# Performance work log

Measured on AMD Instinct MI355X. Metric: run time of the kernel, lower is better.

The kernel has to match this reference:

```python
import jax, jax.numpy as jnp
import numpy as np
from jax import lax

B, N, M = 4, 16384, 512
RADIUS2 = 4.0        # radius=2 (hard-coded in forward), compare squared distances
BALL_K = 64          # k=64 hard-coded in forward
KNN_K = 9            # opt.node_knn_k_1
SIGMA_LB = 0.001     # opt.loss_sigma_lower_bound

_DIMS = [("conv1", 6, 64), ("conv2", 64, 64), ("conv3", 64, 64),
         ("conv4", 128, 128), ("conv5", 128, 128),
         ("knnb1", 131, 256), ("knnb2", 256, 256), ("knnb3", 256, 256),
         ("knna1", 512, 512), ("knna2", 512, 512),
         ("mlp1", 640, 512), ("mlp2", 512, 256)]


def setup_inputs() -> dict:
    key = jax.random.key(0)
    ks = jax.random.split(key, 6)
    inp = {
        "x": jax.random.normal(ks[0], (B, 3, N), jnp.float32),
        "sn": jax.random.normal(ks[1], (B, 3, N), jnp.float32),
        "node": jax.random.normal(ks[2], (B, 3, M), jnp.float32),
    }
    for i, (name, cin, cout) in enumerate(_DIMS):
        k = jax.random.fold_in(ks[3], i)
        inp[name + "_w"] = jax.random.normal(k, (cout, cin), jnp.float32) * np.float32(1.0 / np.sqrt(cin))
        inp[name + "_b"] = jnp.zeros((cout,), jnp.float32)
    inp["mlp3_w"] = jax.random.normal(ks[4], (4, 256), jnp.float32) * np.float32(1e-4)  # .normal_(0, 0.0001)
    inp["mlp3_b"] = jnp.zeros((4,), jnp.float32)
    return inp


def _conv(f, w, b, act=True):
    # 1x1 conv over (B,C,M) or (B,C,M,K): channel matmul + bias (+relu)
    y = jnp.einsum('oc,bc...->bo...', w, f) + b.reshape((1, -1) + (1,) * (f.ndim - 2))
    return jax.nn.relu(y) if act else y


def _sqdist(a, b):
    # a: (B,3,Ma), b: (B,3,Nb) -> (B,Ma,Nb) squared euclidean distances
    aa = jnp.sum(a * a, axis=1)
    bb = jnp.sum(b * b, axis=1)
    ab = jnp.einsum('bcm,bcn->bmn', a, b)
    return aa[:, :, None] + bb[:, None, :] - 2.0 * ab


def _gather(feat, idx):
    # feat: (B,C,Nb), idx: (B,Mq,K) -> (B,C,Mq,K)
    Bq, C, _ = feat.shape
    _, Mq, K = idx.shape
    flat = jnp.broadcast_to(idx.reshape(Bq, 1, Mq * K), (Bq, C, Mq * K))
    return jnp.take_along_axis(feat, flat, axis=2).reshape(Bq, C, Mq, K)


def _ball_query(sqd, radius2, k):
    # first k point indices (in original order) with dist<radius, padded by the first hit
    n = sqd.shape[2]
    mask = sqd < radius2
    keyi = jnp.where(mask, jnp.arange(n, dtype=jnp.int32)[None, None, :], jnp.int32(n))
    _, idx = lax.top_k(-keyi, k)  # k smallest keys == first k in-ball indices
    count = jnp.sum(mask, axis=2, keepdims=True)
    return jnp.where(jnp.arange(k)[None, None, :] < count, idx, idx[:, :, :1])


def reference(x, sn, node,
              conv1_w, conv1_b, conv2_w, conv2_b, conv3_w, conv3_b,
              conv4_w, conv4_b, conv5_w, conv5_b,
              knnb1_w, knnb1_b, knnb2_w, knnb2_b, knnb3_w, knnb3_b,
              knna1_w, knna1_b, knna2_w, knna2_b,
              mlp1_w, mlp1_b, mlp2_w, mlp2_b, mlp3_w, mlp3_b):
    x_aug = jnp.concatenate([x, sn], axis=1)                      # (B,6,N)
    idx = _ball_query(_sqdist(node, x), RADIUS2, BALL_K)          # (B,M,64)
    xb = _gather(x_aug, idx)                                      # (B,6,M,64)
    xb = jnp.concatenate([xb[:, :3] - node[:, :, :, None], xb[:, 3:]], axis=1)
    f = _conv(_conv(_conv(xb, conv1_w, conv1_b), conv2_w, conv2_b), conv3_w, conv3_b)
    fmax = jnp.max(f, axis=3, keepdims=True)
    f = jnp.concatenate([f, jnp.broadcast_to(fmax, f.shape)], axis=1)
    f = _conv(_conv(f, conv4_w, conv4_b), conv5_w, conv5_b)
    feat1 = jnp.max(f, axis=3)                                    # (B,128,M)

    # GeneralKNNFusionModule: query=node, database=node, x=feat1, K=KNN_K
    _, knn_idx = lax.top_k(-_sqdist(node, node), KNN_K)           # (B,M,K) nearest nodes
    coords = _gather(node, knn_idx) - node[:, :, :, None]         # (B,3,M,K)
    g = jnp.concatenate([coords, _gather(feat1, knn_idx)], axis=1)  # (B,131,M,K)
    g = _conv(_conv(_conv(g, knnb1_w, knnb1_b), knnb2_w, knnb2_b), knnb3_w, knnb3_b)
    gmax = jnp.max(g, axis=3, keepdims=True)
    g = jnp.concatenate([g, jnp.broadcast_to(gmax, g.shape)], axis=1)
    g = _conv(_conv(g, knna1_w, knna1_b), knna2_w, knna2_b)
    feat2 = jnp.max(g, axis=3)                                    # (B,512,M)

    h = jnp.concatenate([feat1, feat2], axis=1)                   # (B,640,M)
    h = _conv(_conv(h, mlp1_w, mlp1_b), mlp2_w, mlp2_b)
    ksig = _conv(h, mlp3_w, mlp3_b, act=False)                    # (B,4,M)
    keypoints = ksig[:, :3] + node
    sigmas = jax.nn.softplus(ksig[:, 3]) + SIGMA_LB
    return node, keypoints, sigmas
```

## Files before the change

### kernel.cpp

```cpp
#include <hip/hip_runtime.h>

typedef unsigned short u16;
typedef unsigned int u32;
typedef __bf16 bf16x8 __attribute__((ext_vector_type(8)));
typedef float floatx4 __attribute__((ext_vector_type(4)));
typedef unsigned short u16x8 __attribute__((ext_vector_type(8)));
typedef unsigned int u32x4 __attribute__((ext_vector_type(4)));

static constexpr int B_ = 4;
static constexpr int N_ = 16384;
static constexpr int M_ = 512;

__device__ __forceinline__ u16 f2bf(float f) {
    u32 u = __float_as_uint(f);
    u32 r = (u + 0x7fffu + ((u >> 16) & 1u)) >> 16;
    return (u16)r;
}
__device__ __forceinline__ float bf2f(u16 x) {
    return __uint_as_float(((u32)x) << 16);
}
__device__ __forceinline__ u32 pack2(float a, float b) {
    return (u32)f2bf(a) | ((u32)f2bf(b) << 16);
}

__global__ void pack_x_kernel(const float* __restrict__ x, float4* __restrict__ pk) {
    int t = blockIdx.x * 256 + threadIdx.x;
    int b = t >> 14, n = t & (N_ - 1);
    const float* xb = x + (size_t)b * 3 * N_;
    float px = xb[n], py = xb[N_ + n], pz = xb[2 * N_ + n];
    pk[t] = make_float4(px, py, pz, px * px + py * py + pz * pz);
}

__global__ __launch_bounds__(256) void ball_query_kernel(
    const float4* __restrict__ pk, const float* __restrict__ node, int* __restrict__ idx) {
    int bm = blockIdx.x;
    int b = bm >> 9, m = bm & 511;
    int tid = threadIdx.x, wave = tid >> 6, lane = tid & 63;
    __shared__ int sidx[4][64];
    __shared__ int scnt[4];

    const float4* pb = pk + ((size_t)b << 14);
    float nx = node[((size_t)b * 3 + 0) * M_ + m];
    float ny = node[((size_t)b * 3 + 1) * M_ + m];
    float nz = node[((size_t)b * 3 + 2) * M_ + m];
    float aa = nx * nx + ny * ny + nz * nz;

    int cnt = 0;
    int base = wave * 4096;
    for (int n0 = base; n0 < base + 4096; n0 += 64) {
        float4 p = pb[n0 + lane];
        float d = aa + p.w - 2.0f * (nx * p.x + ny * p.y + nz * p.z);
        bool inb = d < 4.0f;
        unsigned long long mask = __ballot(inb);
        if (inb && cnt < 64) {
            int pos = cnt + __popcll(mask & ((1ull << lane) - 1ull));
            if (pos < 64) sidx[wave][pos] = n0 + lane;
        }
        cnt += __popcll(mask);
        if (cnt >= 64) break;
    }
    if (lane == 0) scnt[wave] = cnt;
    __syncthreads();
    if (tid < 64) {
        int total = scnt[0] + scnt[1] + scnt[2] + scnt[3];
        int v = 0;
        if (total > 0) {
            int lim = total < 64 ? total : 64;
            int slot = tid < lim ? tid : 0;
            int w = 0, pre = 0;
            while (w < 3 && slot >= pre + scnt[w]) { pre += scnt[w]; ++w; }
            v = sidx[w][slot - pre];
        }
        idx[(size_t)bm * 64 + tid] = v;
    }
}

__global__ void knn_kernel(const float* __restrict__ node, int* __restrict__ knn) {
    int bm = blockIdx.x;
    int b = bm >> 9, m = bm & 511;
    int lane = threadIdx.x;
    const float* nb = node + (size_t)b * 3 * M_;
    float nx = nb[m], ny = nb[M_ + m], nz = nb[2 * M_ + m];
    float aa = nx * nx + ny * ny + nz * nz;

    float dist[8];
    int didx[8];
#pragma unroll
    for (int i = 0; i < 8; ++i) {
        int n = lane + i * 64;
        float px = nb[n], py = nb[M_ + n], pz = nb[2 * M_ + n];
        float bb = px * px + py * py + pz * pz;
        float ab = nx * px + ny * py + nz * pz;
        dist[i] = aa + bb - 2.0f * ab;
        didx[i] = n;
    }
    for (int r = 0; r < 9; ++r) {
        float bv = dist[0]; int bi = didx[0]; int bslot = 0;
#pragma unroll
        for (int i = 1; i < 8; ++i) {
            if (dist[i] < bv || (dist[i] == bv && didx[i] < bi)) {
                bv = dist[i]; bi = didx[i]; bslot = i;
            }
        }
        float rv = bv; int ri = bi;
        for (int off = 32; off > 0; off >>= 1) {
            float ov = __shfl_down(rv, off);
            int   oi = __shfl_down(ri, off);
            if (ov < rv || (ov == rv && oi < ri)) { rv = ov; ri = oi; }
        }
        ri = __shfl(ri, 0);
        if (lane == 0) knn[(size_t)bm * 9 + r] = ri;
        if (bi == ri) dist[bslot] = 3.0e38f;
    }
}

struct WConvArgs { const float* src[12]; };

__global__ void convert_weights_kernel(WConvArgs args, u16* __restrict__ dst) {
    const int CI[12] = {6, 64, 64, 128, 128, 131, 256, 256, 512, 512, 640, 512};
    const int KP[12] = {32, 64, 64, 128, 128, 160, 256, 256, 512, 512, 640, 512};
    const int OFF[13] = {0, 2048, 6144, 10240, 26624, 43008, 83968, 149504,
                         215040, 477184, 739328, 1067008, 1198080};
    int e = blockIdx.x * 256 + threadIdx.x;
    if (e >= 1198080) return;
    int w = 0;
    while (e >= OFF[w + 1]) ++w;
    int local = e - OFF[w];
    int kp = KP[w];
    int co = local / kp, k = local - co * kp;
    float v = 0.0f;
    if (w == 5) {
        if (k < 3) v = args.src[5][(size_t)co * 131 + k];
        else if (k >= 8 && k < 136) v = args.src[5][(size_t)co * 131 + (k - 5)];
    } else if (k < CI[w]) {
        v = args.src[w][(size_t)co * CI[w] + k];
    }
    dst[e] = f2bf(v);
}

static constexpr int RS = 136;

__device__ __forceinline__ bf16x8 ldsA(const u16* act, int rf, int l15, int quad, int ks) {
    return *(const bf16x8*)(act + (rf * 16 + l15) * RS + ks * 32 + quad * 8);
}
__device__ __forceinline__ bf16x8 ldW(const u16* W, int ks, int l15, int quad, int kstride) {
    return *(const bf16x8*)(W + (size_t)l15 * kstride + ks * 32 + quad * 8);
}

__global__ __launch_bounds__(256, 2) void fused_stage1_kernel(
    const float* __restrict__ x, const float* __restrict__ sn,
    const float* __restrict__ node, const int* __restrict__ idx,
    const u16* __restrict__ Wbf,
    const float* __restrict__ b1, const float* __restrict__ b2,
    const float* __restrict__ b3, const float* __restrict__ b4,
    const float* __restrict__ b5, u16* __restrict__ h) {
    __shared__ __align__(16) u16 act[128 * RS];
    __shared__ __align__(16) u16 mv[2][64];
    int blk = blockIdx.x;
    int bm0 = blk * 2;
    int tid = threadIdx.x, wave = tid >> 6, lane = tid & 63;
    int quad = lane >> 4, l15 = lane & 15;

    {
        int row = tid & 127, grp = tid >> 7;
        int bm = bm0 + (row >> 6);
        int b = bm >> 9, m = bm & 511;
        int j = idx[(size_t)bm * 64 + (row & 63)];
        const float* xb = x + (size_t)b * 3 * N_;
        const float* sb = sn + (size_t)b * 3 * N_;
        u16* r = act + row * RS;
        if (grp == 0) {
            float c0 = xb[j]          - node[((size_t)b * 3 + 0) * M_ + m];
            float c1 = xb[N_ + j]     - node[((size_t)b * 3 + 1) * M_ + m];
            float c2 = xb[2 * N_ + j] - node[((size_t)b * 3 + 2) * M_ + m];
            *(u32*)(r)     = pack2(c0, c1);
            *(u32*)(r + 2) = pack2(c2, sb[j]);
        } else {
            *(u32*)(r + 4) = pack2(sb[N_ + j], sb[2 * N_ + j]);
            *(u32*)(r + 6) = 0u;
            u32x4* z = (u32x4*)(r + 8);
            z[0] = (u32x4){0u, 0u, 0u, 0u};
            z[1] = (u32x4){0u, 0u, 0u, 0u};
            z[2] = (u32x4){0u, 0u, 0u, 0u};
        }
    }
    __syncthreads();

    {
        const u16* Wp = Wbf + (size_t)(wave * 16) * 32;
        bf16x8 bw = ldW(Wp, 0, l15, quad, 32);
        floatx4 c[8];
#pragma unroll
        for (int rf = 0; rf < 8; ++rf) {
            bf16x8 a = ldsA(act, rf, l15, quad, 0);
            c[rf] = __builtin_amdgcn_mfma_f32_16x16x32_bf16(a, bw, (floatx4){0.f,0.f,0.f,0.f}, 0, 0, 0);
        }
        float bias = b1[wave * 16 + l15];
        __syncthreads();
#pragma unroll
        for (int rf = 0; rf < 8; ++rf)
#pragma unroll
            for (int r = 0; r < 4; ++r)
                act[(rf * 16 + quad * 4 + r) * RS + wave * 16 + l15] = f2bf(fmaxf(c[rf][r] + bias, 0.0f));
        __syncthreads();
    }

    const int WOFF23[2] = {2048, 6144};
    const float* bp23[2] = {b2, b3};
#pragma unroll 1
    for (int cv = 0; cv < 2; ++cv) {
        const u16* Wp = Wbf + WOFF23[cv] + (size_t)(wave * 16) * 64;
        bf16x8 bw0 = ldW(Wp, 0, l15, quad, 64);
        bf16x8 bw1 = ldW(Wp, 1, l15, quad, 64);
        floatx4 c[8] = {};
#pragma unroll
        for (int ks = 0; ks < 2; ++ks)
#pragma unroll
            for (int rf = 0; rf < 8; ++rf) {
                bf16x8 a = ldsA(act, rf, l15, quad, ks);
                c[rf] = __builtin_amdgcn_mfma_f32_16x16x32_bf16(a, ks ? bw1 : bw0, c[rf], 0, 0, 0);
            }
        float bias = bp23[cv][wave * 16 + l15];
        float mxA = 0.0f, mxB = 0.0f;
#pragma unroll
        for (int rf = 0; rf < 8; ++rf)
#pragma unroll
            for (int r = 0; r < 4; ++r) {
                float v = fmaxf(c[rf][r] + bias, 0.0f);
                if (rf < 4) mxA = fmaxf(mxA, v); else mxB = fmaxf(mxB, v);
            }
        __syncthreads();
#pragma unroll
        for (int rf = 0; rf < 8; ++rf)
#pragma unroll
            for (int r = 0; r < 4; ++r)
                act[(rf * 16 + quad * 4 + r) * RS + wave * 16 + l15] = f2bf(fmaxf(c[rf][r] + bias, 0.0f));
        if (cv == 1) {
            mxA = fmaxf(mxA, __shfl_xor(mxA, 16));
            mxA = fmaxf(mxA, __shfl_xor(mxA, 32));
            mxB = fmaxf(mxB, __shfl_xor(mxB, 16));
            mxB = fmaxf(mxB, __shfl_xor(mxB, 32));
            if (quad == 0) {
                mv[0][wave * 16 + l15] = f2bf(mxA);
                mv[1][wave * 16 + l15] = f2bf(mxB);
            }
        }
        __syncthreads();
    }

    {
        const u16* Wp = Wbf + 10240 + (size_t)(wave * 32) * 128;
        bf16x8 bw[2][4];
#pragma unroll
        for (int cf = 0; cf < 2; ++cf)
#pragma unroll
            for (int ks = 0; ks < 4; ++ks)
                bw[cf][ks] = ldW(Wp + (size_t)cf * 16 * 128, ks, l15, quad, 128);
        floatx4 c[8][2] = {};
#pragma unroll
        for (int ks = 0; ks < 4; ++ks)
#pragma unroll
            for (int rf = 0; rf < 8; ++rf) {
                bf16x8 a = (ks < 2) ? ldsA(act, rf, l15, quad, ks)
                                    : *(const bf16x8*)(&mv[rf >> 2][(ks - 2) * 32 + quad * 8]);
#pragma unroll
                for (int cf = 0; cf < 2; ++cf)
                    c[rf][cf] = __builtin_amdgcn_mfma_f32_16x16x32_bf16(a, bw[cf][ks], c[rf][cf], 0, 0, 0);
            }
        float bias[2];
#pragma unroll
        for (int cf = 0; cf < 2; ++cf) bias[cf] = b4[wave * 32 + cf * 16 + l15];
        __syncthreads();
#pragma unroll
        for (int rf = 0; rf < 8; ++rf)
#pragma unroll
            for (int cf = 0; cf < 2; ++cf)
#pragma unroll
                for (int r = 0; r < 4; ++r)
                    act[(rf * 16 + quad * 4 + r) * RS + wave * 32 + cf * 16 + l15] =
                        f2bf(fmaxf(c[rf][cf][r] + bias[cf], 0.0f));
        __syncthreads();
    }

    {
        const u16* Wp = Wbf + 26624 + (size_t)(wave * 32) * 128;
        bf16x8 bw[2][4];
#pragma unroll
        for (int cf = 0; cf < 2; ++cf)
#pragma unroll
            for (int ks = 0; ks < 4; ++ks)
                bw[cf][ks] = ldW(Wp + (size_t)cf * 16 * 128, ks, l15, quad, 128);
        floatx4 c[8][2] = {};
#pragma unroll
        for (int ks = 0; ks < 4; ++ks)
#pragma unroll
            for (int rf = 0; rf < 8; ++rf) {
                bf16x8 a = ldsA(act, rf, l15, quad, ks);
#pragma unroll
                for (int cf = 0; cf < 2; ++cf)
                    c[rf][cf] = __builtin_amdgcn_mfma_f32_16x16x32_bf16(a, bw[cf][ks], c[rf][cf], 0, 0, 0);
            }
#pragma unroll
        for (int cf = 0; cf < 2; ++cf) {
            float bias = b5[wave * 32 + cf * 16 + l15];
            float mxA = 0.0f, mxB = 0.0f;
#pragma unroll
            for (int rf = 0; rf < 8; ++rf)
#pragma unroll
                for (int r = 0; r < 4; ++r) {
                    float v = fmaxf(c[rf][cf][r] + bias, 0.0f);
                    if (rf < 4) mxA = fmaxf(mxA, v); else mxB = fmaxf(mxB, v);
                }
            mxA = fmaxf(mxA, __shfl_xor(mxA, 16));
            mxA = fmaxf(mxA, __shfl_xor(mxA, 32));
            mxB = fmaxf(mxB, __shfl_xor(mxB, 16));
            mxB = fmaxf(mxB, __shfl_xor(mxB, 32));
            if (quad == 0) {
                h[(size_t)bm0 * 640 + wave * 32 + cf * 16 + l15] = f2bf(mxA);
                h[(size_t)(bm0 + 1) * 640 + wave * 32 + cf * 16 + l15] = f2bf(mxB);
            }
        }
    }
}

template <int KS, int CF, int RF, int RSx>
__device__ __forceinline__ void conv_inplace(u16* act, const u16* __restrict__ W0, int KP,
                                             const float* __restrict__ bias, int cb,
                                             int l15, int quad) {
    floatx4 acc[RF][CF];
#pragma unroll
    for (int rf = 0; rf < RF; ++rf)
#pragma unroll
        for (int cf = 0; cf < CF; ++cf) acc[rf][cf] = (floatx4){0.f, 0.f, 0.f, 0.f};

    bf16x8 bwA[CF], bwB[CF];
#pragma unroll
    for (int cf = 0; cf < CF; ++cf)
        bwA[cf] = *(const bf16x8*)(W0 + (size_t)(cb + cf * 16 + l15) * KP + quad * 8);

#pragma unroll
    for (int ks = 0; ks < KS; ++ks) {
        bf16x8* cur = (ks % 2 == 0) ? bwA : bwB;
        bf16x8* nxt = (ks % 2 == 0) ? bwB : bwA;
        if (ks + 1 < KS) {
#pragma unroll
            for (int cf = 0; cf < CF; ++cf)
                nxt[cf] = *(const bf16x8*)(W0 + (size_t)(cb + cf * 16 + l15) * KP +
                                           (ks + 1) * 32 + quad * 8);
        }
#pragma unroll
        for (int rf = 0; rf < RF; ++rf) {
            bf16x8 a = *(const bf16x8*)(act + (rf * 16 + l15) * RSx + ks * 32 + quad * 8);
#pragma unroll
            for (int cf = 0; cf < CF; ++cf)
                acc[rf][cf] = __builtin_amdgcn_mfma_f32_16x16x32_bf16(a, cur[cf], acc[rf][cf], 0, 0, 0);
        }
    }
    __syncthreads();
#pragma unroll
    for (int cf = 0; cf < CF; ++cf) {
        float bs = bias[cb + cf * 16 + l15];
#pragma unroll
        for (int rf = 0; rf < RF; ++rf)
#pragma unroll
            for (int r = 0; r < 4; ++r)
                act[(rf * 16 + quad * 4 + r) * RSx + cb + cf * 16 + l15] =
                    f2bf(fmaxf(acc[rf][cf][r] + bs, 0.0f));
    }
    __syncthreads();
}

static constexpr int RS2 = 520;

__global__ __launch_bounds__(1024, 4) void fused_stage2_kernel(
    const float* __restrict__ node, u16* __restrict__ h, const int* __restrict__ knn,
    const u16* __restrict__ Wbf,
    const float* __restrict__ bb1, const float* __restrict__ bb2,
    const float* __restrict__ bb3, const float* __restrict__ ba1,
    const float* __restrict__ ba2) {
    __shared__ __align__(16) u16 act[80 * RS2];
    int blk = blockIdx.x;
    int node0 = blk * 8;
    int b = node0 >> 9;
    int tid = threadIdx.x, wave = tid >> 6, lane = tid & 63;
    int quad = lane >> 4, l15 = lane & 15;
    (void)lane;

    for (int e = tid; e < 80 * 20; e += 1024)
        *(u16x8*)(act + (e / 20) * RS2 + (e % 20) * 8) = (u16x8){0,0,0,0,0,0,0,0};
    __syncthreads();
    for (int e = tid; e < 72 * 3; e += 1024) {
        int r = e / 3, c = e - r * 3;
        int nodei = node0 + r / 9;
        int j = knn[(size_t)nodei * 9 + (r % 9)];
        float v = node[((size_t)b * 3 + c) * M_ + j] - node[((size_t)b * 3 + c) * M_ + (nodei & 511)];
        act[r * RS2 + c] = f2bf(v);
    }
    for (int e = tid; e < 72 * 16; e += 1024) {
        int r = e >> 4, s = e & 15;
        int nodei = node0 + r / 9;
        int j = knn[(size_t)nodei * 9 + (r % 9)];
        *(u16x8*)(act + r * RS2 + 8 + s * 8) =
            *(const u16x8*)(h + (size_t)(b * 512 + j) * 640 + s * 8);
    }
    __syncthreads();

    conv_inplace<5, 1, 5, RS2>(act, Wbf + 43008, 160, bb1, wave * 16, l15, quad);
    conv_inplace<8, 1, 5, RS2>(act, Wbf + 83968, 256, bb2, wave * 16, l15, quad);
    conv_inplace<8, 1, 5, RS2>(act, Wbf + 149504, 256, bb3, wave * 16, l15, quad);

    for (int e = tid; e < 8 * 32; e += 1024) {
        int li = e >> 5, s = e & 31;
        int r0 = li * 9;
        float mx[8];
#pragma unroll
        for (int i = 0; i < 8; ++i) mx[i] = -3.0e38f;
#pragma unroll
        for (int kk = 0; kk < 9; ++kk) {
            u16x8 v = *(const u16x8*)(act + (r0 + kk) * RS2 + s * 8);
#pragma unroll
            for (int i = 0; i < 8; ++i) mx[i] = fmaxf(mx[i], bf2f(v[i]));
        }
        u16x8 o;
#pragma unroll
        for (int i = 0; i < 8; ++i) o[i] = f2bf(mx[i]);
#pragma unroll
        for (int kk = 0; kk < 9; ++kk)
            *(u16x8*)(act + (r0 + kk) * RS2 + 256 + s * 8) = o;
    }
    __syncthreads();

    conv_inplace<16, 2, 5, RS2>(act, Wbf + 215040, 512, ba1, wave * 32, l15, quad);
    conv_inplace<16, 2, 5, RS2>(act, Wbf + 477184, 512, ba2, wave * 32, l15, quad);

    for (int e = tid; e < 8 * 64; e += 1024) {
        int li = e >> 6, s = e & 63;
        int r0 = li * 9;
        float mx[8];
#pragma unroll
        for (int i = 0; i < 8; ++i) mx[i] = -3.0e38f;
#pragma unroll
        for (int kk = 0; kk < 9; ++kk) {
            u16x8 v = *(const u16x8*)(act + (r0 + kk) * RS2 + s * 8);
#pragma unroll
            for (int i = 0; i < 8; ++i) mx[i] = fmaxf(mx[i], bf2f(v[i]));
        }
        u16x8 o;
#pragma unroll
        for (int i = 0; i < 8; ++i) o[i] = f2bf(mx[i]);
        *(u16x8*)(h + (size_t)(node0 + li) * 640 + 128 + s * 8) = o;
    }
}

static constexpr int RS3 = 648;

__global__ __launch_bounds__(512, 2) void fused_stage3_kernel(
    const float* __restrict__ node, const u16* __restrict__ h,
    const u16* __restrict__ Wbf,
    const float* __restrict__ bm1, const float* __restrict__ bm2,
    const float* __restrict__ w3, const float* __restrict__ b3,
    float* __restrict__ out) {
    __shared__ __align__(16) u16 act[16 * RS3];
    int blk = blockIdx.x;
    int node0 = blk * 8;
    int tid = threadIdx.x, lane = tid & 63, wave = tid >> 6;
    int quad = lane >> 4, l15 = lane & 15;

    for (int e = tid; e < 16 * 80; e += 512) {
        int r = e / 80, seg = e - r * 80;
        u16x8 v = (r < 8) ? *(const u16x8*)(h + (size_t)(node0 + r) * 640 + seg * 8)
                          : (u16x8){0,0,0,0,0,0,0,0};
        *(u16x8*)(act + r * RS3 + seg * 8) = v;
    }
    __syncthreads();

    conv_inplace<20, 4, 1, RS3>(act, Wbf + 739328, 640, bm1, wave * 64, l15, quad);
    conv_inplace<16, 2, 1, RS3>(act, Wbf + 1067008, 512, bm2, wave * 32, l15, quad);

    if (tid < 32) {
        int li = tid >> 2, oc = tid & 3;
        const u16* row = act + li * RS3;
        const float* wrow = w3 + oc * 256;
        float a = 0.0f;
        for (int c = 0; c < 256; c += 4) {
            a += bf2f(row[c]) * wrow[c];
            a += bf2f(row[c + 1]) * wrow[c + 1];
            a += bf2f(row[c + 2]) * wrow[c + 2];
            a += bf2f(row[c + 3]) * wrow[c + 3];
        }
        a += b3[oc];
        int nodei = node0 + li;
        int b = nodei >> 9, m = nodei & 511;
        if (oc < 3) {
            float nv = node[((size_t)b * 3 + oc) * M_ + m];
            out[((size_t)b * 3 + oc) * M_ + m] = nv;
            out[6144 + ((size_t)b * 3 + oc) * M_ + m] = nv + a;
        } else {
            out[12288 + nodei] = fmaxf(a, 0.0f) + log1pf(expf(-fabsf(a))) + 0.001f;
        }
    }
}

extern "C" void kernel_launch(void* const* d_in, const int* in_sizes, int n_in,
                              void* d_out, int out_size, void* d_ws, size_t ws_size,
                              hipStream_t stream) {
    (void)in_sizes; (void)n_in; (void)out_size; (void)ws_size;
    const float* x = (const float*)d_in[0];
    const float* sn = (const float*)d_in[1];
    const float* node = (const float*)d_in[2];
    const float* W[13];
    const float* Bs[13];
    for (int i = 0; i < 13; ++i) {
        W[i] = (const float*)d_in[3 + 2 * i];
        Bs[i] = (const float*)d_in[4 + 2 * i];
    }
    float* out = (float*)d_out;

    char* ws = (char*)d_ws;
    int* idx = (int*)(ws + 0);
    int* knn = (int*)(ws + 524288);
    u16* Wbf = (u16*)(ws + 598016);
    u16* h   = (u16*)(ws + 2994176);
    float4* pk = (float4*)(ws + 5615616);

    WConvArgs wa;
    for (int w = 0; w < 12; ++w) wa.src[w] = W[w];
    convert_weights_kernel<<<(1198080 + 255) / 256, 256, 0, stream>>>(wa, Wbf);

    pack_x_kernel<<<256, 256, 0, stream>>>(x, pk);
    ball_query_kernel<<<2048, 256, 0, stream>>>(pk, node, idx);
    knn_kernel<<<2048, 64, 0, stream>>>(node, knn);

    fused_stage1_kernel<<<1024, 256, 0, stream>>>(x, sn, node, idx, Wbf,
                                                  Bs[0], Bs[1], Bs[2], Bs[3], Bs[4], h);
    fused_stage2_kernel<<<256, 1024, 0, stream>>>(node, h, knn, Wbf,
                                                  Bs[5], Bs[6], Bs[7], Bs[8], Bs[9]);
    fused_stage3_kernel<<<256, 512, 0, stream>>>(node, h, Wbf, Bs[10], Bs[11],
                                                 W[12], Bs[12], out);
}
```

Before: 257.6 us.

## Merge preprocessing kernels into one launch and deepen weight prefetch pipeline

```diff
diff --git a/kernel.cpp b/kernel.cpp
--- a/kernel.cpp
+++ b/kernel.cpp
@@ -23,119 +23,110 @@
     return (u32)f2bf(a) | ((u32)f2bf(b) << 16);
 }
 
-__global__ void pack_x_kernel(const float* __restrict__ x, float4* __restrict__ pk) {
-    int t = blockIdx.x * 256 + threadIdx.x;
-    int b = t >> 14, n = t & (N_ - 1);
-    const float* xb = x + (size_t)b * 3 * N_;
-    float px = xb[n], py = xb[N_ + n], pz = xb[2 * N_ + n];
-    pk[t] = make_float4(px, py, pz, px * px + py * py + pz * pz);
-}
-
-__global__ __launch_bounds__(256) void ball_query_kernel(
-    const float4* __restrict__ pk, const float* __restrict__ node, int* __restrict__ idx) {
-    int bm = blockIdx.x;
-    int b = bm >> 9, m = bm & 511;
+struct WConvArgs { const float* src[12]; };
+
+__global__ __launch_bounds__(256) void prep_kernel(
+    const float* __restrict__ x, const float* __restrict__ node,
+    int* __restrict__ idx, int* __restrict__ knn,
+    WConvArgs wa, u16* __restrict__ Wbf) {
+    int bid = blockIdx.x;
     int tid = threadIdx.x, wave = tid >> 6, lane = tid & 63;
-    __shared__ int sidx[4][64];
-    __shared__ int scnt[4];
-
-    const float4* pb = pk + ((size_t)b << 14);
-    float nx = node[((size_t)b * 3 + 0) * M_ + m];
-    float ny = node[((size_t)b * 3 + 1) * M_ + m];
-    float nz = node[((size_t)b * 3 + 2) * M_ + m];
-    float aa = nx * nx + ny * ny + nz * nz;
-
-    int cnt = 0;
-    int base = wave * 4096;
-    for (int n0 = base; n0 < base + 4096; n0 += 64) {
-        float4 p = pb[n0 + lane];
-        float d = aa + p.w - 2.0f * (nx * p.x + ny * p.y + nz * p.z);
-        bool inb = d < 4.0f;
-        unsigned long long mask = __ballot(inb);
-        if (inb && cnt < 64) {
-            int pos = cnt + __popcll(mask & ((1ull << lane) - 1ull));
-            if (pos < 64) sidx[wave][pos] = n0 + lane;
-        }
-        cnt += __popcll(mask);
-        if (cnt >= 64) break;
-    }
-    if (lane == 0) scnt[wave] = cnt;
-    __syncthreads();
-    if (tid < 64) {
-        int total = scnt[0] + scnt[1] + scnt[2] + scnt[3];
-        int v = 0;
-        if (total > 0) {
-            int lim = total < 64 ? total : 64;
-            int slot = tid < lim ? tid : 0;
-            int w = 0, pre = 0;
-            while (w < 3 && slot >= pre + scnt[w]) { pre += scnt[w]; ++w; }
-            v = sidx[w][slot - pre];
-        }
-        idx[(size_t)bm * 64 + tid] = v;
-    }
-}
-
-__global__ void knn_kernel(const float* __restrict__ node, int* __restrict__ knn) {
-    int bm = blockIdx.x;
-    int b = bm >> 9, m = bm & 511;
-    int lane = threadIdx.x;
-    const float* nb = node + (size_t)b * 3 * M_;
-    float nx = nb[m], ny = nb[M_ + m], nz = nb[2 * M_ + m];
-    float aa = nx * nx + ny * ny + nz * nz;
-
-    float dist[8];
-    int didx[8];
-#pragma unroll
-    for (int i = 0; i < 8; ++i) {
-        int n = lane + i * 64;
-        float px = nb[n], py = nb[M_ + n], pz = nb[2 * M_ + n];
-        float bb = px * px + py * py + pz * pz;
-        float ab = nx * px + ny * py + nz * pz;
-        dist[i] = aa + bb - 2.0f * ab;
-        didx[i] = n;
-    }
-    for (int r = 0; r < 9; ++r) {
-        float bv = dist[0]; int bi = didx[0]; int bslot = 0;
-#pragma unroll
-        for (int i = 1; i < 8; ++i) {
-            if (dist[i] < bv || (dist[i] == bv && didx[i] < bi)) {
-                bv = dist[i]; bi = didx[i]; bslot = i;
-            }
-        }
-        float rv = bv; int ri = bi;
-        for (int off = 32; off > 0; off >>= 1) {
-            float ov = __shfl_down(rv, off);
-            int   oi = __shfl_down(ri, off);
-            if (ov < rv || (ov == rv && oi < ri)) { rv = ov; ri = oi; }
-        }
-        ri = __shfl(ri, 0);
-        if (lane == 0) knn[(size_t)bm * 9 + r] = ri;
-        if (bi == ri) dist[bslot] = 3.0e38f;
-    }
-}
-
-struct WConvArgs { const float* src[12]; };
-
-__global__ void convert_weights_kernel(WConvArgs args, u16* __restrict__ dst) {
-    const int CI[12] = {6, 64, 64, 128, 128, 131, 256, 256, 512, 512, 640, 512};
-    const int KP[12] = {32, 64, 64, 128, 128, 160, 256, 256, 512, 512, 640, 512};
-    const int OFF[13] = {0, 2048, 6144, 10240, 26624, 43008, 83968, 149504,
-                         215040, 477184, 739328, 1067008, 1198080};
-    int e = blockIdx.x * 256 + threadIdx.x;
-    if (e >= 1198080) return;
-    int w = 0;
-    while (e >= OFF[w + 1]) ++w;
-    int local = e - OFF[w];
-    int kp = KP[w];
-    int co = local / kp, k = local - co * kp;
-    float v = 0.0f;
-    if (w == 5) {
-        if (k < 3) v = args.src[5][(size_t)co * 131 + k];
-        else if (k >= 8 && k < 136) v = args.src[5][(size_t)co * 131 + (k - 5)];
-    } else if (k < CI[w]) {
-        v = args.src[w][(size_t)co * CI[w] + k];
-    }
-    dst[e] = f2bf(v);
+
+    if (bid < 2048) {
+        int bm = bid;
+        int b = bm >> 9, m = bm & 511;
+        __shared__ int sidx[4][64];
+        __shared__ int scnt[4];
+        const float* xb = x + (size_t)b * 3 * N_;
+        float nx = node[((size_t)b * 3 + 0) * M_ + m];
+        float ny = node[((size_t)b * 3 + 1) * M_ + m];
+        float nz = node[((size_t)b * 3 + 2) * M_ + m];
+        float aa = nx * nx + ny * ny + nz * nz;
+        int cnt = 0;
+        int base = wave * 4096;
+        for (int n0 = base; n0 < base + 4096; n0 += 64) {
+            int n = n0 + lane;
+            float px = xb[n], py = xb[N_ + n], pz = xb[2 * N_ + n];
+            float w = px * px + py * py + pz * pz;
+            float d = aa + w - 2.0f * (nx * px + ny * py + nz * pz);
+            bool inb = d < 4.0f;
+            unsigned long long mask = __ballot(inb);
+            if (inb && cnt < 64) {
+                int pos = cnt + __popcll(mask & ((1ull << lane) - 1ull));
+                if (pos < 64) sidx[wave][pos] = n;
+            }
+            cnt += __popcll(mask);
+            if (cnt >= 64) break;
+        }
+        if (lane == 0) scnt[wave] = cnt;
+        __syncthreads();
+        if (tid < 64) {
+            int total = scnt[0] + scnt[1] + scnt[2] + scnt[3];
+            int v = 0;
+            if (total > 0) {
+                int lim = total < 64 ? total : 64;
+                int slot = tid < lim ? tid : 0;
+                int w = 0, pre = 0;
+                while (w < 3 && slot >= pre + scnt[w]) { pre += scnt[w]; ++w; }
+                v = sidx[w][slot - pre];
+            }
+            idx[(size_t)bm * 64 + tid] = v;
+        }
+    } else if (bid < 2560) {
+        int bm = (bid - 2048) * 4 + wave;
+        int b = bm >> 9, m = bm & 511;
+        const float* nb = node + (size_t)b * 3 * M_;
+        float nx = nb[m], ny = nb[M_ + m], nz = nb[2 * M_ + m];
+        float aa = nx * nx + ny * ny + nz * nz;
+        float dist[8];
+        int didx[8];
+#pragma unroll
+        for (int i = 0; i < 8; ++i) {
+            int n = lane + i * 64;
+            float px = nb[n], py = nb[M_ + n], pz = nb[2 * M_ + n];
+            float bb = px * px + py * py + pz * pz;
+            float ab = nx * px + ny * py + nz * pz;
+            dist[i] = aa + bb - 2.0f * ab;
+            didx[i] = n;
+        }
+        for (int r = 0; r < 9; ++r) {
+            float bv = dist[0]; int bi = didx[0]; int bslot = 0;
+#pragma unroll
+            for (int i = 1; i < 8; ++i) {
+                if (dist[i] < bv || (dist[i] == bv && didx[i] < bi)) {
+                    bv = dist[i]; bi = didx[i]; bslot = i;
+                }
+            }
+            float rv = bv; int ri = bi;
+            for (int off = 32; off > 0; off >>= 1) {
+                float ov = __shfl_down(rv, off);
+                int   oi = __shfl_down(ri, off);
+                if (ov < rv || (ov == rv && oi < ri)) { rv = ov; ri = oi; }
+            }
+            ri = __shfl(ri, 0);
+            if (lane == 0) knn[(size_t)bm * 9 + r] = ri;
+            if (bi == ri) dist[bslot] = 3.0e38f;
+        }
+    } else {
+        const int CI[12] = {6, 64, 64, 128, 128, 131, 256, 256, 512, 512, 640, 512};
+        const int KP[12] = {32, 64, 64, 128, 128, 160, 256, 256, 512, 512, 640, 512};
+        const int OFF[13] = {0, 2048, 6144, 10240, 26624, 43008, 83968, 149504,
+                             215040, 477184, 739328, 1067008, 1198080};
+        int e = (bid - 2560) * 256 + tid;
+        int w = 0;
+        while (e >= OFF[w + 1]) ++w;
+        int local = e - OFF[w];
+        int kp = KP[w];
+        int co = local / kp, k = local - co * kp;
+        float v = 0.0f;
+        if (w == 5) {
+            if (k < 3) v = wa.src[5][(size_t)co * 131 + k];
+            else if (k >= 8 && k < 136) v = wa.src[5][(size_t)co * 131 + (k - 5)];
+        } else if (k < CI[w]) {
+            v = wa.src[w][(size_t)co * CI[w] + k];
+        }
+        Wbf[e] = f2bf(v);
+    }
 }
 
 static constexpr int RS = 136;
@@ -147,7 +138,7 @@
     return *(const bf16x8*)(W + (size_t)l15 * kstride + ks * 32 + quad * 8);
 }
 
-__global__ __launch_bounds__(256, 2) void fused_stage1_kernel(
+__global__ __launch_bounds__(256, 3) void fused_stage1_kernel(
     const float* __restrict__ x, const float* __restrict__ sn,
     const float* __restrict__ node, const int* __restrict__ idx,
     const u16* __restrict__ Wbf,
@@ -333,27 +324,29 @@
 #pragma unroll
         for (int cf = 0; cf < CF; ++cf) acc[rf][cf] = (floatx4){0.f, 0.f, 0.f, 0.f};
 
-    bf16x8 bwA[CF], bwB[CF];
-#pragma unroll
-    for (int cf = 0; cf < CF; ++cf)
-        bwA[cf] = *(const bf16x8*)(W0 + (size_t)(cb + cf * 16 + l15) * KP + quad * 8);
+    bf16x8 bw[4][CF];
+#pragma unroll
+    for (int p = 0; p < 3; ++p)
+        if (p < KS)
+#pragma unroll
+            for (int cf = 0; cf < CF; ++cf)
+                bw[p][cf] = *(const bf16x8*)(W0 + (size_t)(cb + cf * 16 + l15) * KP +
+                                             p * 32 + quad * 8);
 
 #pragma unroll
     for (int ks = 0; ks < KS; ++ks) {
-        bf16x8* cur = (ks % 2 == 0) ? bwA : bwB;
-        bf16x8* nxt = (ks % 2 == 0) ? bwB : bwA;
-        if (ks + 1 < KS) {
+        if (ks + 3 < KS) {
 #pragma unroll
             for (int cf = 0; cf < CF; ++cf)
-                nxt[cf] = *(const bf16x8*)(W0 + (size_t)(cb + cf * 16 + l15) * KP +
-                                           (ks + 1) * 32 + quad * 8);
+                bw[(ks + 3) & 3][cf] = *(const bf16x8*)(W0 + (size_t)(cb + cf * 16 + l15) * KP +
+                                                        (ks + 3) * 32 + quad * 8);
         }
 #pragma unroll
         for (int rf = 0; rf < RF; ++rf) {
             bf16x8 a = *(const bf16x8*)(act + (rf * 16 + l15) * RSx + ks * 32 + quad * 8);
 #pragma unroll
             for (int cf = 0; cf < CF; ++cf)
-                acc[rf][cf] = __builtin_amdgcn_mfma_f32_16x16x32_bf16(a, cur[cf], acc[rf][cf], 0, 0, 0);
+                acc[rf][cf] = __builtin_amdgcn_mfma_f32_16x16x32_bf16(a, bw[ks & 3][cf], acc[rf][cf], 0, 0, 0);
         }
     }
     __syncthreads();
@@ -521,15 +514,11 @@
     int* knn = (int*)(ws + 524288);
     u16* Wbf = (u16*)(ws + 598016);
     u16* h   = (u16*)(ws + 2994176);
-    float4* pk = (float4*)(ws + 5615616);
 
     WConvArgs wa;
     for (int w = 0; w < 12; ++w) wa.src[w] = W[w];
-    convert_weights_kernel<<<(1198080 + 255) / 256, 256, 0, stream>>>(wa, Wbf);
-
-    pack_x_kernel<<<256, 256, 0, stream>>>(x, pk);
-    ball_query_kernel<<<2048, 256, 0, stream>>>(pk, node, idx);
-    knn_kernel<<<2048, 64, 0, stream>>>(node, knn);
+
+    prep_kernel<<<7240, 256, 0, stream>>>(x, node, idx, knn, wa, Wbf);
 
     fused_stage1_kernel<<<1024, 256, 0, stream>>>(x, sn, node, idx, Wbf,
                                                   Bs[0], Bs[1], Bs[2], Bs[3], Bs[4], h);
```

After: 248.8 us. -3.4%, faster.
